# Optimization experiments

Hardware: AMD Instinct MI355X
Metric: run time of the kernel (lower is better)

## Reference

```python
import jax, jax.numpy as jnp
import numpy as np

N, E, D, C, A, OUT, H = 50000, 800000, 64, 3, 1, 128, 8
NEG_SLOPE = 0.01  # torch LeakyReLU default


def leaky_relu(v):
    return jnp.where(v >= 0, v, NEG_SLOPE * v)


def setup_inputs() -> dict:
    key = jax.random.key(0)
    ks = jax.random.split(key, 12)
    x = jax.random.normal(ks[0], (N, D), dtype=jnp.float32)
    edge_index = jax.random.randint(ks[1], (2, E), 0, N, dtype=jnp.int64)
    edge_attr = jax.random.uniform(ks[2], (E, A), dtype=jnp.float32)
    s = 0.1
    return {
        "x": x,
        "edge_index": edge_index,
        "edge_attr": edge_attr,
        # per-channel edge MLP: A -> 8 -> 1
        "w1": jax.random.normal(ks[3], (C, A, H), dtype=jnp.float32) * s,
        "b1": jnp.zeros((C, H), dtype=jnp.float32),
        "w2": jax.random.normal(ks[4], (C, H, 1), dtype=jnp.float32) * s,
        "b2": jnp.zeros((C, 1), dtype=jnp.float32),
        "eps": jnp.zeros((C,), dtype=jnp.float32),
        # output MLP: C*D -> OUT -> OUT
        "nn_w1": jax.random.normal(ks[5], (C * D, OUT), dtype=jnp.float32) * s,
        "nn_b1": jnp.zeros((OUT,), dtype=jnp.float32),
        "nn_w2": jax.random.normal(ks[6], (OUT, OUT), dtype=jnp.float32) * s,
        "nn_b2": jnp.zeros((OUT,), dtype=jnp.float32),
    }


def reference(x, edge_index, edge_attr, w1, b1, w2, b2, eps,
              nn_w1, nn_b1, nn_w2, nn_b2):
    src, dst = edge_index[0], edge_index[1]
    # per-channel scalar edge weight from tiny MLP: [C, E, 1]
    h = leaky_relu(jnp.einsum('ea,cah->ceh', edge_attr, w1) + b1[:, None, :])
    w = jax.nn.elu(jnp.einsum('ceh,cho->ceo', h, w2) + b2[:, None, :])
    # gather source node features once: [E, D]
    x_j = x[src]
    # weighted messages [E, C, D], scatter-add over destination nodes
    msg = x_j[:, None, :] * jnp.transpose(w, (1, 0, 2))  # [E, C, 1] broadcast
    agg = jax.ops.segment_sum(msg, dst, num_segments=N)  # [N, C, D]
    # residual: out_c += (1 + eps_c) * x
    out = agg + (1.0 + eps)[None, :, None] * x[:, None, :]
    # concat channels along feature dim -> [N, C*D]
    out = out.reshape(N, C * D)
    # final MLP
    out = leaky_relu(out @ nn_w1 + nn_b1)
    out = out @ nn_w2 + nn_b2
    return out
```

## Files before the change

kernel.cpp:

```cpp
#include <hip/hip_runtime.h>
#include <math.h>

#define N_NODES 50000
#define E_EDGES 800000
#define D_FEAT  64
#define C_CH    3
#define H_HID   8
#define OUT_F   128
#define CD      192
#define NTILES  (N_NODES / 16)
#define XCVT_BLOCKS (N_NODES * D_FEAT / 4 / 256)
#define EDGEB   ((E_EDGES + 1023) / 1024)
#define NBUCK   196
#define BCAP    5120

typedef _Float16 half8 __attribute__((ext_vector_type(8)));
typedef _Float16 half4 __attribute__((ext_vector_type(4)));
typedef float f32x4 __attribute__((ext_vector_type(4)));

__device__ __forceinline__ float lrelu(float v) { return v >= 0.f ? v : 0.01f * v; }

__device__ __forceinline__ unsigned short f2h_bits(float f) {
    _Float16 h = (_Float16)f;
    unsigned short b;
    __builtin_memcpy(&b, &h, 2);
    return b;
}
__device__ __forceinline__ float h2f_bits(unsigned b) {
    unsigned short s = (unsigned short)b;
    _Float16 h;
    __builtin_memcpy(&h, &s, 2);
    return (float)h;
}

__device__ __forceinline__ float edge_mlp(
    float a, const float* __restrict__ w1, const float* __restrict__ b1,
    const float* __restrict__ w2, float b2c, int c)
{
    float s = 0.f;
#pragma unroll
    for (int h = 0; h < H_HID; ++h) {
        float t = fmaf(a, w1[c * H_HID + h], b1[c * H_HID + h]);
        t = (t >= 0.f) ? t : 0.01f * t;
        s = fmaf(t, w2[c * H_HID + h], s);
    }
    s += b2c;
    return (s > 0.f) ? s : expm1f(s);
}

__global__ __launch_bounds__(256) void k_part(
    const float* __restrict__ x, _Float16* __restrict__ xh,
    const int* __restrict__ ei, const float* __restrict__ ea,
    const float* __restrict__ w1, const float* __restrict__ b1,
    const float* __restrict__ w2, const float* __restrict__ b2,
    int* __restrict__ bcnt, uint2* __restrict__ brec,
    unsigned char* __restrict__ bd8)
{
    if (blockIdx.x >= EDGEB) {
        int i = (blockIdx.x - EDGEB) * 256 + threadIdx.x;
        float4 f = ((const float4*)x)[i];
        half4 h;
        h[0] = (_Float16)f.x; h[1] = (_Float16)f.y;
        h[2] = (_Float16)f.z; h[3] = (_Float16)f.w;
        *(half4*)(xh + (size_t)i * 4) = h;
        return;
    }
    __shared__ int hist[256];
    __shared__ int gbase[256];

    const int tid = threadIdx.x;
    const int e0  = blockIdx.x * 1024 + tid * 4;
    const int* dstp = ei + E_EDGES;
    const float b20 = b2[0], b21 = b2[1], b22 = b2[2];

    hist[tid] = 0;
    __syncthreads();

    int   sv[4], de[4];
    float av[4];
    if (e0 + 3 < E_EDGES) {
        int4   s4 = *(const int4*)(ei + e0);
        int4   d4 = *(const int4*)(dstp + e0);
        float4 a4 = *(const float4*)(ea + e0);
        sv[0]=s4.x; sv[1]=s4.y; sv[2]=s4.z; sv[3]=s4.w;
        de[0]=d4.x; de[1]=d4.y; de[2]=d4.z; de[3]=d4.w;
        av[0]=a4.x; av[1]=a4.y; av[2]=a4.z; av[3]=a4.w;
    } else {
#pragma unroll
        for (int j = 0; j < 4; ++j) {
            int e = e0 + j;
            sv[j] = (e < E_EDGES) ? ei[e]   : 0;
            de[j] = (e < E_EDGES) ? dstp[e] : -1;
            av[j] = (e < E_EDGES) ? ea[e]   : 0.f;
        }
    }

    int bk[4], lr[4];
#pragma unroll
    for (int j = 0; j < 4; ++j) {
        if (de[j] >= 0) {
            bk[j] = de[j] >> 8;
            lr[j] = atomicAdd(&hist[bk[j]], 1);
        } else bk[j] = -1;
    }
    __syncthreads();
    if (tid < NBUCK && hist[tid]) gbase[tid] = atomicAdd(bcnt + tid, hist[tid]);
    __syncthreads();

#pragma unroll
    for (int j = 0; j < 4; ++j) {
        if (bk[j] >= 0) {
            float w0 = edge_mlp(av[j], w1, b1, w2, b20, 0);
            float wA = edge_mlp(av[j], w1, b1, w2, b21, 1);
            float wB = edge_mlp(av[j], w1, b1, w2, b22, 2);
            uint2 r;
            r.x = (unsigned)sv[j] | ((unsigned)f2h_bits(w0) << 16);
            r.y = (unsigned)f2h_bits(wA) | ((unsigned)f2h_bits(wB) << 16);
            int pos = gbase[bk[j]] + lr[j];
            brec[(size_t)bk[j] * BCAP + pos] = r;
            bd8 [(size_t)bk[j] * BCAP + pos] = (unsigned char)(de[j] & 255);
        }
    }
}

__global__ __launch_bounds__(256) void k_sortb(
    const int* __restrict__ bcnt, const uint2* __restrict__ brec,
    const unsigned char* __restrict__ bd8,
    int* __restrict__ offsets, uint2* __restrict__ sorted)
{
    __shared__ int sc[256];
    __shared__ int nodeh[256];
    __shared__ int pfx[256];
    __shared__ int cursor[256];
    __shared__ unsigned char s8[BCAP];

    const int tid = threadIdx.x;
    const int b   = blockIdx.x;

    sc[tid]    = (tid < NBUCK) ? bcnt[tid] : 0;
    nodeh[tid] = 0;
    __syncthreads();
    for (int off = 1; off < 256; off <<= 1) {
        int t = (tid >= off) ? sc[tid - off] : 0;
        __syncthreads();
        sc[tid] += t;
        __syncthreads();
    }
    const int base = (b == 0) ? 0 : sc[b - 1];
    const int cnt  = bcnt[b];

    for (int i = tid; i < cnt; i += 256) {
        unsigned char d = bd8[(size_t)b * BCAP + i];
        s8[i] = d;
        atomicAdd(&nodeh[d], 1);
    }
    __syncthreads();

    pfx[tid] = nodeh[tid];
    __syncthreads();
    for (int off = 1; off < 256; off <<= 1) {
        int t = (tid >= off) ? pfx[tid - off] : 0;
        __syncthreads();
        pfx[tid] += t;
        __syncthreads();
    }
    const int excl = pfx[tid] - nodeh[tid];
    cursor[tid] = excl;
    int n = b * 256 + tid;
    if (n < N_NODES) offsets[n] = base + excl;
    __syncthreads();

    for (int i = tid; i < cnt; i += 256) {
        uint2 r = brec[(size_t)b * BCAP + i];
        int pos = atomicAdd(&cursor[s8[i]], 1);
        sorted[base + pos] = r;
    }
}

__global__ __launch_bounds__(256) void k_gather(
    const uint2* __restrict__ sorted, const int* __restrict__ offsets,
    const _Float16* __restrict__ xh, const float* __restrict__ eps,
    _Float16* __restrict__ v)
{
    const int n    = blockIdx.x * 4 + (threadIdx.x >> 6);
    const int lane = threadIdx.x & 63;

    const int start = offsets[n];
    const int end   = (n + 1 < N_NODES) ? offsets[n + 1] : E_EDGES;

    float xn = (float)xh[(size_t)n * D_FEAT + lane];

    float a0 = 0.f, a1 = 0.f, a2 = 0.f;
    float b0 = 0.f, b1 = 0.f, b2 = 0.f;
    float c0 = 0.f, c1 = 0.f, c2 = 0.f;
    float d0 = 0.f, d1 = 0.f, d2 = 0.f;

    for (int base = start; base < end; base += 64) {
        const int m = min(64, end - base);
        uint2 rec = make_uint2(0u, 0u);
        if (lane < m) rec = sorted[base + lane];
        int j = 0;
        for (; j + 4 <= m; j += 4) {
            unsigned rxA = (unsigned)__shfl((int)rec.x, j);
            unsigned ryA = (unsigned)__shfl((int)rec.y, j);
            unsigned rxB = (unsigned)__shfl((int)rec.x, j + 1);
            unsigned ryB = (unsigned)__shfl((int)rec.y, j + 1);
            unsigned rxC = (unsigned)__shfl((int)rec.x, j + 2);
            unsigned ryC = (unsigned)__shfl((int)rec.y, j + 2);
            unsigned rxD = (unsigned)__shfl((int)rec.x, j + 3);
            unsigned ryD = (unsigned)__shfl((int)rec.y, j + 3);
            float xA = (float)xh[(size_t)(rxA & 0xFFFFu) * D_FEAT + lane];
            float xB = (float)xh[(size_t)(rxB & 0xFFFFu) * D_FEAT + lane];
            float xC = (float)xh[(size_t)(rxC & 0xFFFFu) * D_FEAT + lane];
            float xD = (float)xh[(size_t)(rxD & 0xFFFFu) * D_FEAT + lane];
            a0 = fmaf(h2f_bits(rxA >> 16),     xA, a0);
            a1 = fmaf(h2f_bits(ryA & 0xFFFFu), xA, a1);
            a2 = fmaf(h2f_bits(ryA >> 16),     xA, a2);
            b0 = fmaf(h2f_bits(rxB >> 16),     xB, b0);
            b1 = fmaf(h2f_bits(ryB & 0xFFFFu), xB, b1);
            b2 = fmaf(h2f_bits(ryB >> 16),     xB, b2);
            c0 = fmaf(h2f_bits(rxC >> 16),     xC, c0);
            c1 = fmaf(h2f_bits(ryC & 0xFFFFu), xC, c1);
            c2 = fmaf(h2f_bits(ryC >> 16),     xC, c2);
            d0 = fmaf(h2f_bits(rxD >> 16),     xD, d0);
            d1 = fmaf(h2f_bits(ryD & 0xFFFFu), xD, d1);
            d2 = fmaf(h2f_bits(ryD >> 16),     xD, d2);
        }
        for (; j < m; ++j) {
            unsigned rx0 = (unsigned)__shfl((int)rec.x, j);
            unsigned ry0 = (unsigned)__shfl((int)rec.y, j);
            float xa = (float)xh[(size_t)(rx0 & 0xFFFFu) * D_FEAT + lane];
            a0 = fmaf(h2f_bits(rx0 >> 16),     xa, a0);
            a1 = fmaf(h2f_bits(ry0 & 0xFFFFu), xa, a1);
            a2 = fmaf(h2f_bits(ry0 >> 16),     xa, a2);
        }
    }
    a0 += b0 + c0 + d0;
    a1 += b1 + c1 + d1;
    a2 += b2 + c2 + d2;

    _Float16* vr = v + (size_t)n * CD;
    vr[lane]       = (_Float16)(a0 + (1.f + eps[0]) * xn);
    vr[64 + lane]  = (_Float16)(a1 + (1.f + eps[1]) * xn);
    vr[128 + lane] = (_Float16)(a2 + (1.f + eps[2]) * xn);
}

__global__ __launch_bounds__(256) void k_mlp(
    const _Float16* __restrict__ v,
    const float* __restrict__ nw1, const float* __restrict__ nb1,
    const float* __restrict__ nw2, const float* __restrict__ nb2,
    float* __restrict__ out)
{
    __shared__ _Float16 vtile[16][CD + 8];
    __shared__ _Float16 htile[16][OUT_F + 8];

    const int tid  = threadIdx.x;
    const int lane = tid & 63;
    const int wid  = tid >> 6;
    const int arow = lane & 15;
    const int kg   = lane >> 4;
    const int o0   = wid * 32;

    half8 w1f[6][2], w2f[4][2];
#pragma unroll
    for (int kk = 0; kk < 6; ++kk)
#pragma unroll
        for (int nt = 0; nt < 2; ++nt) {
            half8 f;
            int colb = o0 + nt * 16 + arow;
            int kb = kk * 32 + kg * 8;
#pragma unroll
            for (int j = 0; j < 8; ++j)
                f[j] = (_Float16)nw1[(size_t)(kb + j) * OUT_F + colb];
            w1f[kk][nt] = f;
        }
#pragma unroll
    for (int kk = 0; kk < 4; ++kk)
#pragma unroll
        for (int nt = 0; nt < 2; ++nt) {
            half8 f;
            int colb = o0 + nt * 16 + arow;
            int kb = kk * 32 + kg * 8;
#pragma unroll
            for (int j = 0; j < 8; ++j)
                f[j] = (_Float16)nw2[(size_t)(kb + j) * OUT_F + colb];
            w2f[kk][nt] = f;
        }

    const float b1a = nb1[o0 + arow],      b1b = nb1[o0 + 16 + arow];
    const float b2a = nb2[o0 + arow],      b2b = nb2[o0 + 16 + arow];

    for (int t = blockIdx.x; t < NTILES; t += gridDim.x) {
        const int nb16 = t * 16;
        __syncthreads();

        for (int i = tid; i < 16 * (CD / 8); i += 256) {
            int row = i / (CD / 8), c8 = i % (CD / 8);
            *(half8*)&vtile[row][c8 * 8] =
                *(const half8*)(v + (size_t)(nb16 + row) * CD + c8 * 8);
        }
        __syncthreads();

        f32x4 acc0 = {0.f, 0.f, 0.f, 0.f}, acc1 = {0.f, 0.f, 0.f, 0.f};
#pragma unroll
        for (int kk = 0; kk < 6; ++kk) {
            half8 a = *(const half8*)&vtile[arow][kk * 32 + kg * 8];
            acc0 = __builtin_amdgcn_mfma_f32_16x16x32_f16(a, w1f[kk][0], acc0, 0, 0, 0);
            acc1 = __builtin_amdgcn_mfma_f32_16x16x32_f16(a, w1f[kk][1], acc1, 0, 0, 0);
        }
#pragma unroll
        for (int r = 0; r < 4; ++r) {
            int hr = kg * 4 + r;
            htile[hr][o0 + arow]      = (_Float16)lrelu(acc0[r] + b1a);
            htile[hr][o0 + 16 + arow] = (_Float16)lrelu(acc1[r] + b1b);
        }
        __syncthreads();

        f32x4 c0 = {0.f, 0.f, 0.f, 0.f}, c1 = {0.f, 0.f, 0.f, 0.f};
#pragma unroll
        for (int kk = 0; kk < 4; ++kk) {
            half8 a = *(const half8*)&htile[arow][kk * 32 + kg * 8];
            c0 = __builtin_amdgcn_mfma_f32_16x16x32_f16(a, w2f[kk][0], c0, 0, 0, 0);
            c1 = __builtin_amdgcn_mfma_f32_16x16x32_f16(a, w2f[kk][1], c1, 0, 0, 0);
        }
#pragma unroll
        for (int r = 0; r < 4; ++r) {
            size_t n = (size_t)(nb16 + kg * 4 + r);
            out[n * OUT_F + o0 + arow]      = c0[r] + b2a;
            out[n * OUT_F + o0 + 16 + arow] = c1[r] + b2b;
        }
    }
}

extern "C" void kernel_launch(void* const* d_in, const int* in_sizes, int n_in,
                              void* d_out, int out_size, void* d_ws, size_t ws_size,
                              hipStream_t stream)
{
    const float* x    = (const float*)d_in[0];
    const int*   ei   = (const int*)  d_in[1];
    const float* ea   = (const float*)d_in[2];
    const float* w1   = (const float*)d_in[3];
    const float* b1   = (const float*)d_in[4];
    const float* w2   = (const float*)d_in[5];
    const float* b2   = (const float*)d_in[6];
    const float* eps  = (const float*)d_in[7];
    const float* nw1  = (const float*)d_in[8];
    const float* nb1  = (const float*)d_in[9];
    const float* nw2  = (const float*)d_in[10];
    const float* nb2  = (const float*)d_in[11];
    float* out = (float*)d_out;

    char* ws = (char*)d_ws;
    int*            bcnt    = (int*)           (ws + 0);
    int*            offsets = (int*)           (ws + 4096);
    uint2*          brec    = (uint2*)         (ws + 212992);
    unsigned char*  bd8     = (unsigned char*) (ws + 8241152);
    uint2*          sorted  = (uint2*)         (ws + 9244672);
    _Float16*       v       = (_Float16*)      (ws + 15644672);

    _Float16* xh = (_Float16*)d_out;

    hipMemsetAsync(bcnt, 0, NBUCK * sizeof(int), stream);

    k_part  <<<EDGEB + XCVT_BLOCKS, 256, 0, stream>>>(
        x, xh, ei, ea, w1, b1, w2, b2, bcnt, brec, bd8);
    k_sortb <<<NBUCK,       256, 0, stream>>>(bcnt, brec, bd8, offsets, sorted);
    k_gather<<<N_NODES / 4, 256, 0, stream>>>(sorted, offsets, xh, eps, v);
    k_mlp   <<<768,         256, 0, stream>>>(v, nw1, nb1, nw2, nb2, out);
}
```

Measured before the change: 94.16 us.

## Fuse bucket sort and gather into one kernel using LDS-resident records

Merges the per-bucket counting sort and the per-node gather into a single kernel. Sorted edge records stay in shared memory instead of round-tripping through a global sorted array and offsets buffer. This removes one launch and the global write and read of the sorted records. In exchange the gather phase runs on only 196 blocks of 1024 threads, with each wave processing 16 nodes serially. That sharply reduces parallelism and the ability to hide gather latency.

Result: slower. 99.03 us (+5.2%).

```diff
diff --git a/kernel.cpp b/kernel.cpp
--- a/kernel.cpp
+++ b/kernel.cpp
@@ -123,126 +123,111 @@
     }
 }
 
-__global__ __launch_bounds__(256) void k_sortb(
+__global__ __launch_bounds__(1024) void k_sg(
     const int* __restrict__ bcnt, const uint2* __restrict__ brec,
     const unsigned char* __restrict__ bd8,
-    int* __restrict__ offsets, uint2* __restrict__ sorted)
-{
-    __shared__ int sc[256];
+    const _Float16* __restrict__ xh, const float* __restrict__ eps,
+    _Float16* __restrict__ v)
+{
+    __shared__ uint2 srec[BCAP];
+    __shared__ unsigned char s8[BCAP];
     __shared__ int nodeh[256];
-    __shared__ int pfx[256];
+    __shared__ int start[256];
     __shared__ int cursor[256];
-    __shared__ unsigned char s8[BCAP];
 
     const int tid = threadIdx.x;
     const int b   = blockIdx.x;
-
-    sc[tid]    = (tid < NBUCK) ? bcnt[tid] : 0;
-    nodeh[tid] = 0;
-    __syncthreads();
-    for (int off = 1; off < 256; off <<= 1) {
-        int t = (tid >= off) ? sc[tid - off] : 0;
-        __syncthreads();
-        sc[tid] += t;
-        __syncthreads();
-    }
-    const int base = (b == 0) ? 0 : sc[b - 1];
-    const int cnt  = bcnt[b];
-
-    for (int i = tid; i < cnt; i += 256) {
+    const int cnt = bcnt[b];
+
+    if (tid < 256) nodeh[tid] = 0;
+    __syncthreads();
+
+    for (int i = tid; i < cnt; i += 1024) {
         unsigned char d = bd8[(size_t)b * BCAP + i];
         s8[i] = d;
         atomicAdd(&nodeh[d], 1);
     }
     __syncthreads();
 
-    pfx[tid] = nodeh[tid];
+    __shared__ int pfx[256];
+    if (tid < 256) pfx[tid] = nodeh[tid];
     __syncthreads();
     for (int off = 1; off < 256; off <<= 1) {
-        int t = (tid >= off) ? pfx[tid - off] : 0;
-        __syncthreads();
-        pfx[tid] += t;
-        __syncthreads();
-    }
-    const int excl = pfx[tid] - nodeh[tid];
-    cursor[tid] = excl;
-    int n = b * 256 + tid;
-    if (n < N_NODES) offsets[n] = base + excl;
-    __syncthreads();
-
-    for (int i = tid; i < cnt; i += 256) {
+        int t = 0;
+        if (tid < 256 && tid >= off) t = pfx[tid - off];
+        __syncthreads();
+        if (tid < 256) pfx[tid] += t;
+        __syncthreads();
+    }
+    if (tid < 256) {
+        int excl = pfx[tid] - nodeh[tid];
+        start[tid]  = excl;
+        cursor[tid] = excl;
+    }
+    __syncthreads();
+
+    for (int i = tid; i < cnt; i += 1024) {
         uint2 r = brec[(size_t)b * BCAP + i];
         int pos = atomicAdd(&cursor[s8[i]], 1);
-        sorted[base + pos] = r;
-    }
-}
-
-__global__ __launch_bounds__(256) void k_gather(
-    const uint2* __restrict__ sorted, const int* __restrict__ offsets,
-    const _Float16* __restrict__ xh, const float* __restrict__ eps,
-    _Float16* __restrict__ v)
-{
-    const int n    = blockIdx.x * 4 + (threadIdx.x >> 6);
-    const int lane = threadIdx.x & 63;
-
-    const int start = offsets[n];
-    const int end   = (n + 1 < N_NODES) ? offsets[n + 1] : E_EDGES;
-
-    float xn = (float)xh[(size_t)n * D_FEAT + lane];
-
-    float a0 = 0.f, a1 = 0.f, a2 = 0.f;
-    float b0 = 0.f, b1 = 0.f, b2 = 0.f;
-    float c0 = 0.f, c1 = 0.f, c2 = 0.f;
-    float d0 = 0.f, d1 = 0.f, d2 = 0.f;
-
-    for (int base = start; base < end; base += 64) {
-        const int m = min(64, end - base);
-        uint2 rec = make_uint2(0u, 0u);
-        if (lane < m) rec = sorted[base + lane];
-        int j = 0;
-        for (; j + 4 <= m; j += 4) {
-            unsigned rxA = (unsigned)__shfl((int)rec.x, j);
-            unsigned ryA = (unsigned)__shfl((int)rec.y, j);
-            unsigned rxB = (unsigned)__shfl((int)rec.x, j + 1);
-            unsigned ryB = (unsigned)__shfl((int)rec.y, j + 1);
-            unsigned rxC = (unsigned)__shfl((int)rec.x, j + 2);
-            unsigned ryC = (unsigned)__shfl((int)rec.y, j + 2);
-            unsigned rxD = (unsigned)__shfl((int)rec.x, j + 3);
-            unsigned ryD = (unsigned)__shfl((int)rec.y, j + 3);
-            float xA = (float)xh[(size_t)(rxA & 0xFFFFu) * D_FEAT + lane];
-            float xB = (float)xh[(size_t)(rxB & 0xFFFFu) * D_FEAT + lane];
-            float xC = (float)xh[(size_t)(rxC & 0xFFFFu) * D_FEAT + lane];
-            float xD = (float)xh[(size_t)(rxD & 0xFFFFu) * D_FEAT + lane];
-            a0 = fmaf(h2f_bits(rxA >> 16),     xA, a0);
-            a1 = fmaf(h2f_bits(ryA & 0xFFFFu), xA, a1);
-            a2 = fmaf(h2f_bits(ryA >> 16),     xA, a2);
-            b0 = fmaf(h2f_bits(rxB >> 16),     xB, b0);
-            b1 = fmaf(h2f_bits(ryB & 0xFFFFu), xB, b1);
-            b2 = fmaf(h2f_bits(ryB >> 16),     xB, b2);
-            c0 = fmaf(h2f_bits(rxC >> 16),     xC, c0);
-            c1 = fmaf(h2f_bits(ryC & 0xFFFFu), xC, c1);
-            c2 = fmaf(h2f_bits(ryC >> 16),     xC, c2);
-            d0 = fmaf(h2f_bits(rxD >> 16),     xD, d0);
-            d1 = fmaf(h2f_bits(ryD & 0xFFFFu), xD, d1);
-            d2 = fmaf(h2f_bits(ryD >> 16),     xD, d2);
-        }
-        for (; j < m; ++j) {
-            unsigned rx0 = (unsigned)__shfl((int)rec.x, j);
-            unsigned ry0 = (unsigned)__shfl((int)rec.y, j);
-            float xa = (float)xh[(size_t)(rx0 & 0xFFFFu) * D_FEAT + lane];
-            a0 = fmaf(h2f_bits(rx0 >> 16),     xa, a0);
-            a1 = fmaf(h2f_bits(ry0 & 0xFFFFu), xa, a1);
-            a2 = fmaf(h2f_bits(ry0 >> 16),     xa, a2);
-        }
-    }
-    a0 += b0 + c0 + d0;
-    a1 += b1 + c1 + d1;
-    a2 += b2 + c2 + d2;
-
-    _Float16* vr = v + (size_t)n * CD;
-    vr[lane]       = (_Float16)(a0 + (1.f + eps[0]) * xn);
-    vr[64 + lane]  = (_Float16)(a1 + (1.f + eps[1]) * xn);
-    vr[128 + lane] = (_Float16)(a2 + (1.f + eps[2]) * xn);
+        srec[pos] = r;
+    }
+    __syncthreads();
+
+    const int w    = tid >> 6;
+    const int lane = tid & 63;
+    const float e0c = 1.f + eps[0], e1c = 1.f + eps[1], e2c = 1.f + eps[2];
+
+    for (int q = 0; q < 16; ++q) {
+        const int slot = w * 16 + q;
+        const int n    = b * 256 + slot;
+        if (n >= N_NODES) break;
+        const int s0 = start[slot];
+        const int s1 = s0 + nodeh[slot];
+
+        float xn = (float)xh[(size_t)n * D_FEAT + lane];
+
+        float a0 = 0.f, a1 = 0.f, a2 = 0.f;
+        float b0 = 0.f, b1 = 0.f, b2 = 0.f;
+        float c0 = 0.f, c1 = 0.f, c2 = 0.f;
+        float d0 = 0.f, d1 = 0.f, d2 = 0.f;
+
+        int i = s0;
+        for (; i + 4 <= s1; i += 4) {
+            uint2 rA = srec[i],     rB = srec[i + 1];
+            uint2 rC = srec[i + 2], rD = srec[i + 3];
+            float xA = (float)xh[(size_t)(rA.x & 0xFFFFu) * D_FEAT + lane];
+            float xB = (float)xh[(size_t)(rB.x & 0xFFFFu) * D_FEAT + lane];
+            float xC = (float)xh[(size_t)(rC.x & 0xFFFFu) * D_FEAT + lane];
+            float xD = (float)xh[(size_t)(rD.x & 0xFFFFu) * D_FEAT + lane];
+            a0 = fmaf(h2f_bits(rA.x >> 16),     xA, a0);
+            a1 = fmaf(h2f_bits(rA.y & 0xFFFFu), xA, a1);
+            a2 = fmaf(h2f_bits(rA.y >> 16),     xA, a2);
+            b0 = fmaf(h2f_bits(rB.x >> 16),     xB, b0);
+            b1 = fmaf(h2f_bits(rB.y & 0xFFFFu), xB, b1);
+            b2 = fmaf(h2f_bits(rB.y >> 16),     xB, b2);
+            c0 = fmaf(h2f_bits(rC.x >> 16),     xC, c0);
+            c1 = fmaf(h2f_bits(rC.y & 0xFFFFu), xC, c1);
+            c2 = fmaf(h2f_bits(rC.y >> 16),     xC, c2);
+            d0 = fmaf(h2f_bits(rD.x >> 16),     xD, d0);
+            d1 = fmaf(h2f_bits(rD.y & 0xFFFFu), xD, d1);
+            d2 = fmaf(h2f_bits(rD.y >> 16),     xD, d2);
+        }
+        for (; i < s1; ++i) {
+            uint2 r = srec[i];
+            float xa = (float)xh[(size_t)(r.x & 0xFFFFu) * D_FEAT + lane];
+            a0 = fmaf(h2f_bits(r.x >> 16),     xa, a0);
+            a1 = fmaf(h2f_bits(r.y & 0xFFFFu), xa, a1);
+            a2 = fmaf(h2f_bits(r.y >> 16),     xa, a2);
+        }
+        a0 += b0 + c0 + d0;
+        a1 += b1 + c1 + d1;
+        a2 += b2 + c2 + d2;
+
+        _Float16* vr = v + (size_t)n * CD;
+        vr[lane]       = (_Float16)(a0 + e0c * xn);
+        vr[64 + lane]  = (_Float16)(a1 + e1c * xn);
+        vr[128 + lane] = (_Float16)(a2 + e2c * xn);
+    }
 }
 
 __global__ __launch_bounds__(256) void k_mlp(
@@ -352,11 +337,9 @@
 
     char* ws = (char*)d_ws;
     int*            bcnt    = (int*)           (ws + 0);
-    int*            offsets = (int*)           (ws + 4096);
-    uint2*          brec    = (uint2*)         (ws + 212992);
-    unsigned char*  bd8     = (unsigned char*) (ws + 8241152);
-    uint2*          sorted  = (uint2*)         (ws + 9244672);
-    _Float16*       v       = (_Float16*)      (ws + 15644672);
+    uint2*          brec    = (uint2*)         (ws + 4096);
+    unsigned char*  bd8     = (unsigned char*) (ws + 8032256);
+    _Float16*       v       = (_Float16*)      (ws + 9035776);
 
     _Float16* xh = (_Float16*)d_out;
 
@@ -364,7 +347,6 @@
 
     k_part  <<<EDGEB + XCVT_BLOCKS, 256, 0, stream>>>(
         x, xh, ei, ea, w1, b1, w2, b2, bcnt, brec, bd8);
-    k_sortb <<<NBUCK,       256, 0, stream>>>(bcnt, brec, bd8, offsets, sorted);
-    k_gather<<<N_NODES / 4, 256, 0, stream>>>(sorted, offsets, xh, eps, v);
+    k_sg    <<<NBUCK,       1024, 0, stream>>>(bcnt, brec, bd8, xh, eps, v);
     k_mlp   <<<768,         256, 0, stream>>>(v, nw1, nb1, nw2, nb2, out);
 }
```
